# Performance work log

Measured on AMD Instinct MI355X. Metric: run time of the kernel, lower is better.

The kernel has to match this reference:

```python
import jax, jax.numpy as jnp
import numpy as np

N, E, H, ED, ND, OUT, L = 40000, 640000, 128, 128, 16, 3, 3


def setup_inputs() -> dict:
    key = jax.random.key(0)
    ks = jax.random.split(key, 16)
    s = 0.05  # weight init scale
    return {
        "x": jax.random.normal(ks[0], (N, ND), jnp.float32),
        "edge_index": jax.random.randint(ks[1], (2, E), 0, N, jnp.int32),
        "edge_attr": jax.random.normal(ks[2], (E, ED), jnp.float32),
        "e2n_W1": jax.random.normal(ks[3], (ED, H), jnp.float32) * s,
        "e2n_b1": jnp.zeros((H,), jnp.float32),
        "e2n_W2": jax.random.normal(ks[4], (H, H), jnp.float32) * s,
        "e2n_b2": jnp.zeros((H,), jnp.float32),
        "edge_W1": jax.random.normal(ks[5], (L, 2 * H + ED, H), jnp.float32) * s,
        "edge_b1": jnp.zeros((L, H), jnp.float32),
        "edge_W2": jax.random.normal(ks[6], (L, H, H), jnp.float32) * s,
        "edge_b2": jnp.zeros((L, H), jnp.float32),
        "node_W": jax.random.normal(ks[7], (L, H, H), jnp.float32) * s,
        "node_b": jnp.zeros((L, H), jnp.float32),
        "out_W1": jax.random.normal(ks[8], (H, H), jnp.float32) * s,
        "out_b1": jnp.zeros((H,), jnp.float32),
        "out_W2": jax.random.normal(ks[9], (H, OUT), jnp.float32) * s,
        "out_b2": jnp.zeros((OUT,), jnp.float32),
    }


def reference(x, edge_index, edge_attr, e2n_W1, e2n_b1, e2n_W2, e2n_b2,
              edge_W1, edge_b1, edge_W2, edge_b2, node_W, node_b,
              out_W1, out_b1, out_W2, out_b2):
    n = x.shape[0]
    src, dst = edge_index[0], edge_index[1]

    # edge_to_node_mlp then per-edge scatter-ADD into node features
    em = jax.nn.relu(edge_attr @ e2n_W1 + e2n_b1) @ e2n_W2 + e2n_b2  # [E,H]
    h = jax.ops.segment_sum(em, dst, num_segments=n)  # [N,H]

    # in-degree for mean aggregation (PyG aggr='mean'; empty nodes -> 0)
    cnt = jax.ops.segment_sum(jnp.ones((src.shape[0],), h.dtype), dst, num_segments=n)
    deg = jnp.maximum(cnt, 1.0)[:, None]  # [N,1]

    for l in range(edge_W1.shape[0]):
        feat = jnp.concatenate([h[dst], h[src], edge_attr], axis=-1)  # [E,2H+ED]
        m = jax.nn.relu(feat @ edge_W1[l] + edge_b1[l]) @ edge_W2[l] + edge_b2[l]
        agg = jax.ops.segment_sum(m, dst, num_segments=n) / deg  # scatter-mean
        h = jax.nn.relu(agg @ node_W[l] + node_b[l])

    return jax.nn.relu(h @ out_W1 + out_b1) @ out_W2 + out_b2  # [N,OUT]
```

## Files before the change

### kernel.cpp

```cpp
#include <hip/hip_runtime.h>
#include <hip/hip_bf16.h>

#define DEVINL __device__ __forceinline__

typedef float f32x4 __attribute__((ext_vector_type(4)));
typedef unsigned short u16x8 __attribute__((ext_vector_type(8)));
typedef __bf16 bf16x8 __attribute__((ext_vector_type(8)));

static constexpr int NN = 40000;
static constexpr int NE = 640000;
static constexpr int H  = 128;
static constexpr int NSCAN = 40;

static constexpr long O_HACC = 0;
static constexpr long O_H16  = 20480000;
static constexpr long O_DEG  = 30720000;
static constexpr long O_WP   = 30880000;
static constexpr long O_HDP  = 31600896;
static constexpr long O_HSP  = 41840896;
static constexpr long O_CNT  = 52080896;
static constexpr long O_LOC  = 52240896;
static constexpr long O_ROWP = 52400896;
static constexpr long O_CURS = 52560912;
static constexpr long O_BSUM = 52720912;
static constexpr long O_PERM = 52721168;
static constexpr long O_SRCS = 55281168;
static constexpr long O_DSTS = 57841168;
static constexpr long O_T16  = 60401168;
static constexpr long O_EA16 = 224241168;
static constexpr long NEED_T1 = O_EA16;
static constexpr long NEED_T2 = O_EA16 + (long)NE * H * 2;

__host__ __device__ inline const unsigned short* wpm(const unsigned short* wp, int m) {
  return wp + m * 16384;
}

DEVINL unsigned short f2bf(float f) {
  unsigned int u = __float_as_uint(f);
  u += 0x7fffu + ((u >> 16) & 1u);
  return (unsigned short)(u >> 16);
}
DEVINL float bf2f(unsigned short u) {
  return __uint_as_float(((unsigned int)u) << 16);
}

DEVINL f32x4 mfma16(u16x8 a, u16x8 b, f32x4 c) {
  return __builtin_amdgcn_mfma_f32_16x16x32_bf16(
      __builtin_bit_cast(bf16x8, a), __builtin_bit_cast(bf16x8, b), c, 0, 0, 0);
}

struct PrepPtrs { const float* p[18]; };

__global__ void prep_all(PrepPtrs pp, unsigned short* __restrict__ wp) {
  constexpr int MODE[18] = {0,1, 0,0,0, 0,0,0, 0,0,0, 1,1,1, 0,0,0, 0};
  int m = blockIdx.y;
  int idx = blockIdx.x * 256 + threadIdx.x;
  if (idx >= 16384) return;
  int j  = idx & 7, l = (idx >> 3) & 63, nb = (idx >> 9) & 7, ks = idx >> 12;
  int hi = l >> 4, lo = l & 15;
  int k = MODE[m] ? (4*ks + hi + 16*j) : (32*ks + 8*hi + j);
  int n = nb*16 + lo;
  wp[m * 16384 + idx] = f2bf(pp.p[m][k*128 + n]);
}

__global__ void hist_k(const int* __restrict__ dst, unsigned* __restrict__ cnt) {
  int e = blockIdx.x * 256 + threadIdx.x;
  atomicAdd(&cnt[dst[e]], 1u);
}

__global__ void scan1_k(const unsigned* __restrict__ cnt, unsigned* __restrict__ loc,
                        unsigned* __restrict__ bsum) {
  __shared__ unsigned sh[256];
  int t = threadIdx.x;
  int base = blockIdx.x * 1024 + t * 4;
  unsigned v[4]; unsigned s = 0;
  #pragma unroll
  for (int j = 0; j < 4; ++j) {
    v[j] = (base + j < NN) ? cnt[base + j] : 0u;
    s += v[j];
  }
  sh[t] = s; __syncthreads();
  #pragma unroll
  for (int off = 1; off < 256; off <<= 1) {
    unsigned y = (t >= off) ? sh[t - off] : 0u;
    __syncthreads();
    sh[t] += y;
    __syncthreads();
  }
  unsigned run = sh[t] - s;
  #pragma unroll
  for (int j = 0; j < 4; ++j) {
    if (base + j < NN) loc[base + j] = run;
    run += v[j];
  }
  if (t == 255) bsum[blockIdx.x] = sh[255];
}

__global__ void scan2_k(unsigned* __restrict__ bsum) {
  int t = threadIdx.x;
  unsigned orig = (t < NSCAN) ? bsum[t] : 0u;
  unsigned v = orig;
  #pragma unroll
  for (int off = 1; off < 64; off <<= 1) {
    unsigned y = __shfl_up(v, off);
    if (t >= off) v += y;
  }
  if (t < NSCAN) bsum[t] = v - orig;
}

__global__ void scan3_k(const unsigned* __restrict__ loc, const unsigned* __restrict__ bsum,
                        const unsigned* __restrict__ cnt, unsigned* __restrict__ rowPtr,
                        unsigned* __restrict__ cursor, float* __restrict__ deg_inv) {
  int i = blockIdx.x * 256 + threadIdx.x;
  if (i < NN) {
    unsigned r = loc[i] + bsum[i >> 10];
    rowPtr[i] = r;
    cursor[i] = r;
    deg_inv[i] = 1.0f / fmaxf((float)cnt[i], 1.0f);
  }
  if (i == NN) rowPtr[NN] = (unsigned)NE;
}

__global__ void scat_k(const int* __restrict__ src, const int* __restrict__ dst,
                       unsigned* __restrict__ cursor, unsigned* __restrict__ perm,
                       int* __restrict__ srcS, int* __restrict__ dstS) {
  int e = blockIdx.x * 256 + threadIdx.x;
  int d = dst[e];
  unsigned pos = atomicAdd(&cursor[d], 1u);
  perm[pos] = (unsigned)e;
  srcS[pos] = src[e];
  dstS[pos] = d;
}

__global__ void cvt_h0(const float* __restrict__ src, unsigned short* __restrict__ dst) {
  long i = ((long)blockIdx.x * 256 + threadIdx.x) * 8;
  f32x4 a = *(const f32x4*)(src + i);
  f32x4 b = *(const f32x4*)(src + i + 4);
  u16x8 t;
  #pragma unroll
  for (int j = 0; j < 4; ++j) { t[j] = f2bf(a[j]); t[4+j] = f2bf(b[j]); }
  *(u16x8*)(dst + i) = t;
}

__global__ __launch_bounds__(256) void node_xform(
    const unsigned short* __restrict__ h16,
    const unsigned short* __restrict__ wpa, const unsigned short* __restrict__ wpb,
    unsigned short* __restrict__ Hdp, unsigned short* __restrict__ Hsp) {
  const int tid = threadIdx.x;
  const int wave = tid >> 6, lane = tid & 63;
  const int hi = lane >> 4, lo = lane & 15;
  const int n0w = blockIdx.x * 256 + wave * 64;

  #pragma unroll
  for (int out = 0; out < 2; ++out) {
    const unsigned short* wp = out ? wpb : wpa;
    unsigned short* dp = out ? Hsp : Hdp;
    f32x4 acc[4][8];
    #pragma unroll
    for (int mf = 0; mf < 4; ++mf)
      #pragma unroll
      for (int nb = 0; nb < 8; ++nb) acc[mf][nb] = (f32x4)(0.0f);
    #pragma unroll
    for (int s = 0; s < 4; ++s) {
      u16x8 a[4];
      #pragma unroll
      for (int mf = 0; mf < 4; ++mf) {
        int n = n0w + 16 * mf + lo; if (n >= NN) n = NN - 1;
        a[mf] = *(const u16x8*)(h16 + (long)n * 128 + s * 32 + hi * 8);
      }
      #pragma unroll
      for (int nb = 0; nb < 8; ++nb) {
        u16x8 b = *(const u16x8*)(wp + ((s * 8 + nb) * 64 + lane) * 8);
        #pragma unroll
        for (int mf = 0; mf < 4; ++mf) acc[mf][nb] = mfma16(a[mf], b, acc[mf][nb]);
      }
    }
    #pragma unroll
    for (int mf = 0; mf < 4; ++mf)
      #pragma unroll
      for (int r = 0; r < 4; ++r) {
        int n = n0w + 16 * mf + 4 * hi + r;
        if (n < NN) {
          u16x8 pack;
          #pragma unroll
          for (int nb = 0; nb < 8; ++nb) pack[nb] = f2bf(acc[mf][nb][r]);
          *(u16x8*)(dp + (long)n * 128 + 8 * lo) = pack;
        }
      }
  }
}

template<int EAM, bool EAST, bool GATH>
__global__ __launch_bounds__(256, 2) void k12_pass(
    const float* __restrict__ ea32, unsigned short* __restrict__ ea16,
    const unsigned* __restrict__ perm,
    const unsigned short* __restrict__ w1p, const unsigned short* __restrict__ w2p,
    const float* __restrict__ b1, const float* __restrict__ b2,
    const unsigned short* __restrict__ Hdp, const unsigned short* __restrict__ Hsp,
    const int* __restrict__ srcS, const int* __restrict__ dstS,
    const float* __restrict__ deg_inv, float* __restrict__ hacc) {
  extern __shared__ char smem[];
  const int tid = threadIdx.x;
  const int wave = tid >> 6, lane = tid & 63;
  const int hi = lane >> 4, lo = lane & 15;

  const int nwg = gridDim.x;
  const int xcd = blockIdx.x & 7, bbase = blockIdx.x >> 3;
  const int qc = nwg >> 3, rc = nwg & 7;
  const int bid = (xcd < rc ? xcd * (qc + 1) : rc * (qc + 1) + (xcd - rc) * qc) + bbase;
  const long e0w = (long)bid * 256 + wave * 64;
  char* sstripe = smem + 65536 + wave * 4096;

  constexpr int LB = (EAM == 0 ? 8 : 4) + (GATH ? 8 : 0);

  unsigned pId[4];
  int dId[4], sId[4];
  float dsc[4];
  #pragma unroll
  for (int mf = 0; mf < 4; ++mf) {
    if (EAM == 0) pId[mf] = perm[e0w + 16 * mf + lo];
    dId[mf] = dstS[e0w + 16 * mf + lo];
    if (GATH) {
      sId[mf] = srcS[e0w + 16 * mf + lo];
      dsc[mf] = deg_inv[dId[mf]];
    }
  }

  float b1v[8], b2v[8];
  #pragma unroll
  for (int nb = 0; nb < 8; ++nb) { b1v[nb] = b1[nb * 16 + lo]; b2v[nb] = b2[nb * 16 + lo]; }

  u16x8 eaA[4], eaB[4], gdA[4], gsA[4], gdB[4], gsB[4];
  f32x4 efA[8], efB[8];

  auto issue = [&](int mf, u16x8 (&ea)[4], f32x4 (&ef)[8],
                   u16x8 (&gd)[4], u16x8 (&gs)[4]) {
    if (EAM == 1) {
      #pragma unroll
      for (int s = 0; s < 4; ++s) {
        const unsigned short* p = ea16 + (e0w + 16 * mf + lo) * 128 + s * 32 + hi * 8;
        asm volatile("global_load_dwordx4 %0, %1, off" : "=&v"(ea[s]) : "v"(p) : "memory");
      }
    } else {
      #pragma unroll
      for (int s = 0; s < 4; ++s) {
        const float* p = ea32 + (long)pId[mf] * 128 + s * 32 + hi * 8;
        asm volatile("global_load_dwordx4 %0, %1, off" : "=&v"(ef[2*s])   : "v"(p)     : "memory");
        asm volatile("global_load_dwordx4 %0, %1, off" : "=&v"(ef[2*s+1]) : "v"(p + 4) : "memory");
      }
    }
    if (GATH) {
      #pragma unroll
      for (int r = 0; r < 4; ++r) {
        int rd = __shfl(dId[mf], 4 * hi + r);
        int rs = __shfl(sId[mf], 4 * hi + r);
        const unsigned short* pd = Hdp + (long)rd * 128 + 8 * lo;
        const unsigned short* ps = Hsp + (long)rs * 128 + 8 * lo;
        asm volatile("global_load_dwordx4 %0, %1, off" : "=&v"(gd[r]) : "v"(pd) : "memory");
        asm volatile("global_load_dwordx4 %0, %1, off" : "=&v"(gs[r]) : "v"(ps) : "memory");
      }
    }
  };

  issue(0, eaA, efA, gdA, gsA);

  {
    const u16x8* g1 = (const u16x8*)w1p;
    u16x8* l1 = (u16x8*)smem;
    #pragma unroll
    for (int i = 0; i < 8; ++i) l1[i * 256 + tid] = g1[i * 256 + tid];
    const u16x8* g2 = (const u16x8*)w2p;
    u16x8* l2 = (u16x8*)(smem + 32768);
    #pragma unroll
    for (int i = 0; i < 8; ++i) l2[i * 256 + tid] = g2[i * 256 + tid];
  }
  __syncthreads();

  float runA = 0.0f, runB = 0.0f, scur = 1.0f;
  int dcur = -1;
  const int cA = 16 * ((2 * lane) & 7) + (lane >> 2);
  const int cB = 16 * ((2 * lane + 1) & 7) + (lane >> 2);

  #pragma unroll
  for (int mf = 0; mf < 4; ++mf) {
    u16x8 (&ea)[4] = (mf & 1) ? eaB : eaA;
    f32x4 (&ef)[8] = (mf & 1) ? efB : efA;
    u16x8 (&gd)[4] = (mf & 1) ? gdB : gdA;
    u16x8 (&gs)[4] = (mf & 1) ? gsB : gsA;
    if (mf < 3)
      issue(mf + 1, (mf & 1) ? eaA : eaB, (mf & 1) ? efA : efB,
            (mf & 1) ? gdA : gdB, (mf & 1) ? gsA : gsB);

    if (EAM == 1) {
      if (GATH) {
        asm volatile("s_waitcnt vmcnt(%12)"
          : "+v"(ea[0]), "+v"(ea[1]), "+v"(ea[2]), "+v"(ea[3]),
            "+v"(gd[0]), "+v"(gd[1]), "+v"(gd[2]), "+v"(gd[3]),
            "+v"(gs[0]), "+v"(gs[1]), "+v"(gs[2]), "+v"(gs[3])
          : "n"(mf < 3 ? LB : 0));
      } else {
        asm volatile("s_waitcnt vmcnt(%4)"
          : "+v"(ea[0]), "+v"(ea[1]), "+v"(ea[2]), "+v"(ea[3])
          : "n"(mf < 3 ? LB : 0));
      }
    } else if (GATH) {
      asm volatile("s_waitcnt vmcnt(%16)"
        : "+v"(ef[0]), "+v"(ef[1]), "+v"(ef[2]), "+v"(ef[3]),
          "+v"(ef[4]), "+v"(ef[5]), "+v"(ef[6]), "+v"(ef[7]),
          "+v"(gd[0]), "+v"(gd[1]), "+v"(gd[2]), "+v"(gd[3]),
          "+v"(gs[0]), "+v"(gs[1]), "+v"(gs[2]), "+v"(gs[3])
        : "n"(mf < 3 ? LB : 0));
    } else {
      asm volatile("s_waitcnt vmcnt(%8)"
        : "+v"(ef[0]), "+v"(ef[1]), "+v"(ef[2]), "+v"(ef[3]),
          "+v"(ef[4]), "+v"(ef[5]), "+v"(ef[6]), "+v"(ef[7])
        : "n"(mf < 3 ? LB : 0));
    }

    if (EAM == 0) {
      #pragma unroll
      for (int s = 0; s < 4; ++s) {
        u16x8 t;
        #pragma unroll
        for (int j = 0; j < 4; ++j) { t[j] = f2bf(ef[2*s][j]); t[4+j] = f2bf(ef[2*s+1][j]); }
        if (EAST)
          *(u16x8*)(ea16 + (e0w + 16 * mf + lo) * 128 + s * 32 + hi * 8) = t;
        ea[s] = t;
      }
    }

    f32x4 acc[8];
    #pragma unroll
    for (int nb = 0; nb < 8; ++nb) acc[nb] = (f32x4)(0.0f);
    #pragma unroll
    for (int s = 0; s < 4; ++s)
      #pragma unroll
      for (int nb = 0; nb < 8; ++nb) {
        u16x8 b = *(const u16x8*)(smem + ((s * 8 + nb) << 10) + (lane << 4));
        acc[nb] = mfma16(ea[s], b, acc[nb]);
      }
    if (GATH) {
      #pragma unroll
      for (int nb = 0; nb < 8; ++nb)
        #pragma unroll
        for (int r = 0; r < 4; ++r)
          acc[nb][r] += bf2f(gd[r][nb]) + bf2f(gs[r][nb]);
    }

    #pragma unroll
    for (int r = 0; r < 4; ++r) {
      int er = 4 * hi + r;
      u16x8 pack;
      #pragma unroll
      for (int nb = 0; nb < 8; ++nb)
        pack[nb] = f2bf(fmaxf(acc[nb][r] + b1v[nb], 0.0f));
      *(u16x8*)(sstripe + er * 256 + ((lo * 16) ^ ((er & 7) << 4))) = pack;
    }

    f32x4 acc2[8];
    #pragma unroll
    for (int nb = 0; nb < 8; ++nb) acc2[nb] = (f32x4)(0.0f);
    #pragma unroll
    for (int s2 = 0; s2 < 4; ++s2) {
      u16x8 a = *(const u16x8*)(sstripe + lo * 256 +
                                (((4 * s2 + hi) * 16) ^ ((lo & 7) << 4)));
      #pragma unroll
      for (int nb = 0; nb < 8; ++nb) {
        u16x8 b = *(const u16x8*)(smem + 32768 + ((s2 * 8 + nb) << 10) + (lane << 4));
        acc2[nb] = mfma16(a, b, acc2[nb]);
      }
    }

    #pragma unroll
    for (int r = 0; r < 4; ++r) {
      int er = 4 * hi + r;
      u16x8 pack;
      #pragma unroll
      for (int nb = 0; nb < 8; ++nb)
        pack[nb] = f2bf(acc2[nb][r] + b2v[nb]);
      *(u16x8*)(sstripe + er * 256 + ((lo * 16) ^ ((er & 7) << 4))) = pack;
    }

    #pragma unroll
    for (int er = 0; er < 16; ++er) {
      int d = __shfl(dId[mf], er);
      float s = GATH ? __shfl(dsc[mf], er) : 1.0f;
      if (d != dcur) {
        if (dcur >= 0) {
          unsafeAtomicAdd(&hacc[(long)dcur * 128 + cA], runA * scur);
          unsafeAtomicAdd(&hacc[(long)dcur * 128 + cB], runB * scur);
        }
        runA = 0.0f; runB = 0.0f; dcur = d; scur = s;
      }
      unsigned pr = *(const unsigned*)(sstripe + er * 256 +
                                       ((lane * 4) ^ ((er & 7) << 4)));
      runA += bf2f((unsigned short)(pr & 0xffffu));
      runB += bf2f((unsigned short)(pr >> 16));
    }
  }
  if (dcur >= 0) {
    unsafeAtomicAdd(&hacc[(long)dcur * 128 + cA], runA * scur);
    unsafeAtomicAdd(&hacc[(long)dcur * 128 + cB], runB * scur);
  }
}

__global__ __launch_bounds__(256) void node_pass(
    const float* __restrict__ agg, const unsigned short* __restrict__ wp,
    const float* __restrict__ bias, unsigned short* __restrict__ h16out) {
  __shared__ char smem[49152];
  const int tid = threadIdx.x;
  const int wave = tid >> 6, lane = tid & 63;
  const int hi = lane >> 4, lo = lane & 15;
  const int n0 = blockIdx.x * 64;
  const int r = tid >> 2, q = tid & 3;

  #pragma unroll
  for (int s = 0; s < 4; ++s) {
    f32x4 f0 = *(const f32x4*)(agg + (long)(n0 + r) * 128 + s * 32 + q * 8);
    f32x4 f1 = *(const f32x4*)(agg + (long)(n0 + r) * 128 + s * 32 + q * 8 + 4);
    u16x8 t;
    #pragma unroll
    for (int j = 0; j < 4; ++j) { t[j] = f2bf(f0[j]); t[4+j] = f2bf(f1[j]); }
    *(u16x8*)(smem + s * 4096 + (((r >> 4) * 64 + q * 16 + (r & 15)) << 4)) = t;
  }
  {
    const u16x8* g = (const u16x8*)wp;
    u16x8* l = (u16x8*)(smem + 16384);
    #pragma unroll
    for (int i = 0; i < 8; ++i) l[i * 256 + tid] = g[i * 256 + tid];
  }
  __syncthreads();

  f32x4 acc[8];
  #pragma unroll
  for (int nb = 0; nb < 8; ++nb) acc[nb] = (f32x4)(0.0f);
  #pragma unroll
  for (int s = 0; s < 4; ++s) {
    u16x8 a = *(const u16x8*)(smem + s * 4096 + wave * 1024 + (lane << 4));
    #pragma unroll
    for (int nb = 0; nb < 8; ++nb) {
      u16x8 b = *(const u16x8*)(smem + 16384 + ((s * 8 + nb) << 10) + (lane << 4));
      acc[nb] = mfma16(a, b, acc[nb]);
    }
  }
  float bv[8];
  #pragma unroll
  for (int nb = 0; nb < 8; ++nb) bv[nb] = bias[nb * 16 + lo];
  #pragma unroll
  for (int nb = 0; nb < 8; ++nb)
    #pragma unroll
    for (int rr = 0; rr < 4; ++rr) {
      int node = n0 + 16 * wave + 4 * hi + rr;
      float v = fmaxf(acc[nb][rr] + bv[nb], 0.0f);
      h16out[(long)node * 128 + nb * 16 + lo] = f2bf(v);
    }
}

__global__ __launch_bounds__(256) void out_pass(
    const unsigned short* __restrict__ h16, const unsigned short* __restrict__ wp,
    const float* __restrict__ ob1, const float* __restrict__ oW2,
    const float* __restrict__ ob2, float* __restrict__ out) {
  __shared__ char smem[49152];
  const int tid = threadIdx.x;
  const int wave = tid >> 6, lane = tid & 63;
  const int hi = lane >> 4, lo = lane & 15;
  const int n0 = blockIdx.x * 64;
  const int r = tid >> 2, q = tid & 3;

  #pragma unroll
  for (int s = 0; s < 4; ++s) {
    u16x8 t = *(const u16x8*)(h16 + (long)(n0 + r) * 128 + s * 32 + q * 8);
    *(u16x8*)(smem + s * 4096 + (((r >> 4) * 64 + q * 16 + (r & 15)) << 4)) = t;
  }
  {
    const u16x8* g = (const u16x8*)wp;
    u16x8* l = (u16x8*)(smem + 16384);
    #pragma unroll
    for (int i = 0; i < 8; ++i) l[i * 256 + tid] = g[i * 256 + tid];
  }
  __syncthreads();

  f32x4 acc[8];
  #pragma unroll
  for (int nb = 0; nb < 8; ++nb) acc[nb] = (f32x4)(0.0f);
  #pragma unroll
  for (int s = 0; s < 4; ++s) {
    u16x8 a = *(const u16x8*)(smem + s * 4096 + wave * 1024 + (lane << 4));
    #pragma unroll
    for (int nb = 0; nb < 8; ++nb) {
      u16x8 b = *(const u16x8*)(smem + 16384 + ((s * 8 + nb) << 10) + (lane << 4));
      acc[nb] = mfma16(a, b, acc[nb]);
    }
  }
  float b1v[8], w2v[8][3];
  #pragma unroll
  for (int nb = 0; nb < 8; ++nb) {
    b1v[nb] = ob1[nb * 16 + lo];
    #pragma unroll
    for (int o = 0; o < 3; ++o) w2v[nb][o] = oW2[(nb * 16 + lo) * 3 + o];
  }
  #pragma unroll
  for (int rr = 0; rr < 4; ++rr) {
    float p0 = 0.f, p1 = 0.f, p2 = 0.f;
    #pragma unroll
    for (int nb = 0; nb < 8; ++nb) {
      float t = fmaxf(acc[nb][rr] + b1v[nb], 0.0f);
      p0 += t * w2v[nb][0]; p1 += t * w2v[nb][1]; p2 += t * w2v[nb][2];
    }
    #pragma unroll
    for (int off = 1; off < 16; off <<= 1) {
      p0 += __shfl_xor(p0, off); p1 += __shfl_xor(p1, off); p2 += __shfl_xor(p2, off);
    }
    if (lo == 0) {
      int node = n0 + 16 * wave + 4 * hi + rr;
      out[(long)node * 3 + 0] = p0 + ob2[0];
      out[(long)node * 3 + 1] = p1 + ob2[1];
      out[(long)node * 3 + 2] = p2 + ob2[2];
    }
  }
}

extern "C" void kernel_launch(void* const* d_in, const int* in_sizes, int n_in,
                              void* d_out, int out_size, void* d_ws, size_t ws_size,
                              hipStream_t stream) {
  const int*   ei     = (const int*)d_in[1];
  const int*   srcIds = ei;
  const int*   dstIds = ei + NE;
  const float* ea     = (const float*)d_in[2];
  const float* e2nb1  = (const float*)d_in[4];
  const float* e2nb2  = (const float*)d_in[6];
  const float* eW1    = (const float*)d_in[7];
  const float* eb1    = (const float*)d_in[8];
  const float* eW2    = (const float*)d_in[9];
  const float* eb2    = (const float*)d_in[10];
  const float* nW     = (const float*)d_in[11];
  const float* nb_    = (const float*)d_in[12];
  const float* ob1    = (const float*)d_in[14];
  const float* oW2    = (const float*)d_in[15];
  const float* ob2    = (const float*)d_in[16];
  float* out = (float*)d_out;

  char* ws = (char*)d_ws;
  float* hacc = (float*)(ws + O_HACC);
  unsigned short* h16 = (unsigned short*)(ws + O_H16);
  float* deg_inv = (float*)(ws + O_DEG);
  unsigned short* wp = (unsigned short*)(ws + O_WP);
  unsigned short* Hdp = (unsigned short*)(ws + O_HDP);
  unsigned short* Hsp = (unsigned short*)(ws + O_HSP);
  unsigned* cnt    = (unsigned*)(ws + O_CNT);
  unsigned* loc    = (unsigned*)(ws + O_LOC);
  unsigned* rowPtr = (unsigned*)(ws + O_ROWP);
  unsigned* cursor = (unsigned*)(ws + O_CURS);
  unsigned* bsum   = (unsigned*)(ws + O_BSUM);
  unsigned* perm   = (unsigned*)(ws + O_PERM);
  int* srcS        = (int*)(ws + O_SRCS);
  int* dstS        = (int*)(ws + O_DSTS);
  unsigned short* ea16 = (unsigned short*)(ws + O_EA16);
  const bool tier2 = ws_size >= (size_t)NEED_T2;

  PrepPtrs pp;
  pp.p[0] = (const float*)d_in[3];
  pp.p[1] = (const float*)d_in[5];
  for (int l = 0; l < 3; ++l) {
    pp.p[2 + 3*l] = eW1 + l * 49152;
    pp.p[3 + 3*l] = eW1 + l * 49152 + 16384;
    pp.p[4 + 3*l] = eW1 + l * 49152 + 32768;
    pp.p[11 + l]  = eW2 + l * 16384;
    pp.p[14 + l]  = nW  + l * 16384;
  }
  pp.p[17] = (const float*)d_in[13];

  prep_all<<<dim3(64, 18), 256, 0, stream>>>(pp, wp);

  hipMemsetAsync(cnt, 0, (size_t)NN * 4, stream);
  hist_k<<<NE / 256, 256, 0, stream>>>(dstIds, cnt);
  scan1_k<<<NSCAN, 256, 0, stream>>>(cnt, loc, bsum);
  scan2_k<<<1, 64, 0, stream>>>(bsum);
  scan3_k<<<(NN + 256) / 256, 256, 0, stream>>>(loc, bsum, cnt, rowPtr, cursor, deg_inv);
  scat_k<<<NE / 256, 256, 0, stream>>>(srcIds, dstIds, cursor, perm, srcS, dstS);

  hipMemsetAsync(hacc, 0, (size_t)NN * H * 4, stream);
  if (tier2)
    k12_pass<0, true, false><<<NE / 256, 256, 81920, stream>>>(
        ea, ea16, perm, wpm(wp, 0), wpm(wp, 1), e2nb1, e2nb2,
        nullptr, nullptr, srcS, dstS, deg_inv, hacc);
  else
    k12_pass<0, false, false><<<NE / 256, 256, 81920, stream>>>(
        ea, nullptr, perm, wpm(wp, 0), wpm(wp, 1), e2nb1, e2nb2,
        nullptr, nullptr, srcS, dstS, deg_inv, hacc);
  cvt_h0<<<NN * H / (256 * 8), 256, 0, stream>>>(hacc, h16);

  for (int l = 0; l < 3; ++l) {
    node_xform<<<(NN + 255) / 256, 256, 0, stream>>>(
        h16, wpm(wp, 2 + 3*l), wpm(wp, 3 + 3*l), Hdp, Hsp);
    hipMemsetAsync(hacc, 0, (size_t)NN * H * 4, stream);
    if (tier2)
      k12_pass<1, false, true><<<NE / 256, 256, 81920, stream>>>(
          ea, ea16, perm, wpm(wp, 4 + 3*l), wpm(wp, 11 + l),
          eb1 + l * 128, eb2 + l * 128, Hdp, Hsp, srcS, dstS, deg_inv, hacc);
    else
      k12_pass<0, false, true><<<NE / 256, 256, 81920, stream>>>(
          ea, nullptr, perm, wpm(wp, 4 + 3*l), wpm(wp, 11 + l),
          eb1 + l * 128, eb2 + l * 128, Hdp, Hsp, srcS, dstS, deg_inv, hacc);
    node_pass<<<NN / 64, 256, 0, stream>>>(hacc, wpm(wp, 14 + l),
                                           nb_ + l * 128, h16);
  }

  out_pass<<<NN / 64, 256, 0, stream>>>(h16, wpm(wp, 17), ob1, oW2, ob2, out);
}
```

Before: 633.3 us.

## Fuse node update with next-layer node transform and fold h0 conversion

```diff
diff --git a/kernel.cpp b/kernel.cpp
--- a/kernel.cpp
+++ b/kernel.cpp
@@ -26,9 +26,7 @@
 static constexpr long O_PERM = 52721168;
 static constexpr long O_SRCS = 55281168;
 static constexpr long O_DSTS = 57841168;
-static constexpr long O_T16  = 60401168;
 static constexpr long O_EA16 = 224241168;
-static constexpr long NEED_T1 = O_EA16;
 static constexpr long NEED_T2 = O_EA16 + (long)NE * H * 2;
 
 __host__ __device__ inline const unsigned short* wpm(const unsigned short* wp, int m) {
@@ -49,10 +47,10 @@
       __builtin_bit_cast(bf16x8, a), __builtin_bit_cast(bf16x8, b), c, 0, 0, 0);
 }
 
-struct PrepPtrs { const float* p[18]; };
+struct PrepPtrs { const float* p[22]; };
 
 __global__ void prep_all(PrepPtrs pp, unsigned short* __restrict__ wp) {
-  constexpr int MODE[18] = {0,1, 0,0,0, 0,0,0, 0,0,0, 1,1,1, 0,0,0, 0};
+  constexpr int MODE[22] = {0,1, 0,0,0, 0,0,0, 0,0,0, 1,1,1, 0,0,0, 0, 1,1,1,1};
   int m = blockIdx.y;
   int idx = blockIdx.x * 256 + threadIdx.x;
   if (idx >= 16384) return;
@@ -132,18 +130,8 @@
   dstS[pos] = d;
 }
 
-__global__ void cvt_h0(const float* __restrict__ src, unsigned short* __restrict__ dst) {
-  long i = ((long)blockIdx.x * 256 + threadIdx.x) * 8;
-  f32x4 a = *(const f32x4*)(src + i);
-  f32x4 b = *(const f32x4*)(src + i + 4);
-  u16x8 t;
-  #pragma unroll
-  for (int j = 0; j < 4; ++j) { t[j] = f2bf(a[j]); t[4+j] = f2bf(b[j]); }
-  *(u16x8*)(dst + i) = t;
-}
-
 __global__ __launch_bounds__(256) void node_xform(
-    const unsigned short* __restrict__ h16,
+    const float* __restrict__ hsrc,
     const unsigned short* __restrict__ wpa, const unsigned short* __restrict__ wpb,
     unsigned short* __restrict__ Hdp, unsigned short* __restrict__ Hsp) {
   const int tid = threadIdx.x;
@@ -151,6 +139,20 @@
   const int hi = lane >> 4, lo = lane & 15;
   const int n0w = blockIdx.x * 256 + wave * 64;
 
+  u16x8 a[4][4];
+  #pragma unroll
+  for (int s = 0; s < 4; ++s)
+    #pragma unroll
+    for (int mf = 0; mf < 4; ++mf) {
+      int n = n0w + 16 * mf + lo; if (n >= NN) n = NN - 1;
+      f32x4 f0 = *(const f32x4*)(hsrc + (long)n * 128 + s * 32 + hi * 8);
+      f32x4 f1 = *(const f32x4*)(hsrc + (long)n * 128 + s * 32 + hi * 8 + 4);
+      u16x8 t;
+      #pragma unroll
+      for (int j = 0; j < 4; ++j) { t[j] = f2bf(f0[j]); t[4+j] = f2bf(f1[j]); }
+      a[s][mf] = t;
+    }
+
   #pragma unroll
   for (int out = 0; out < 2; ++out) {
     const unsigned short* wp = out ? wpb : wpa;
@@ -161,20 +163,13 @@
       #pragma unroll
       for (int nb = 0; nb < 8; ++nb) acc[mf][nb] = (f32x4)(0.0f);
     #pragma unroll
-    for (int s = 0; s < 4; ++s) {
-      u16x8 a[4];
-      #pragma unroll
-      for (int mf = 0; mf < 4; ++mf) {
-        int n = n0w + 16 * mf + lo; if (n >= NN) n = NN - 1;
-        a[mf] = *(const u16x8*)(h16 + (long)n * 128 + s * 32 + hi * 8);
-      }
+    for (int s = 0; s < 4; ++s)
       #pragma unroll
       for (int nb = 0; nb < 8; ++nb) {
         u16x8 b = *(const u16x8*)(wp + ((s * 8 + nb) * 64 + lane) * 8);
         #pragma unroll
-        for (int mf = 0; mf < 4; ++mf) acc[mf][nb] = mfma16(a[mf], b, acc[mf][nb]);
-      }
-    }
+        for (int mf = 0; mf < 4; ++mf) acc[mf][nb] = mfma16(a[s][mf], b, acc[mf][nb]);
+      }
     #pragma unroll
     for (int mf = 0; mf < 4; ++mf)
       #pragma unroll
@@ -187,6 +182,106 @@
           *(u16x8*)(dp + (long)n * 128 + 8 * lo) = pack;
         }
       }
+  }
+}
+
+template<bool XF>
+__global__ __launch_bounds__(256) void node_fused(
+    const float* __restrict__ agg, const unsigned short* __restrict__ wn,
+    const float* __restrict__ bias,
+    const unsigned short* __restrict__ w1aK, const unsigned short* __restrict__ w1bK,
+    unsigned short* __restrict__ h16out,
+    unsigned short* __restrict__ Hdp, unsigned short* __restrict__ Hsp) {
+  __shared__ char smem[16384];
+  const int tid = threadIdx.x;
+  const int wave = tid >> 6, lane = tid & 63;
+  const int hi = lane >> 4, lo = lane & 15;
+  const int n0w = blockIdx.x * 256 + wave * 64;
+  char* sstripe = smem + wave * 4096;
+
+  float bv[8];
+  #pragma unroll
+  for (int nb = 0; nb < 8; ++nb) bv[nb] = bias[nb * 16 + lo];
+
+  f32x4 acc[4][8];
+  #pragma unroll
+  for (int mf = 0; mf < 4; ++mf)
+    #pragma unroll
+    for (int nb = 0; nb < 8; ++nb) acc[mf][nb] = (f32x4)(0.0f);
+
+  #pragma unroll
+  for (int s = 0; s < 4; ++s) {
+    u16x8 a[4];
+    #pragma unroll
+    for (int mf = 0; mf < 4; ++mf) {
+      int n = n0w + 16 * mf + lo; if (n >= NN) n = NN - 1;
+      f32x4 f0 = *(const f32x4*)(agg + (long)n * 128 + s * 32 + hi * 8);
+      f32x4 f1 = *(const f32x4*)(agg + (long)n * 128 + s * 32 + hi * 8 + 4);
+      u16x8 t;
+      #pragma unroll
+      for (int j = 0; j < 4; ++j) { t[j] = f2bf(f0[j]); t[4+j] = f2bf(f1[j]); }
+      a[mf] = t;
+    }
+    #pragma unroll
+    for (int nb = 0; nb < 8; ++nb) {
+      u16x8 b = *(const u16x8*)(wn + ((s * 8 + nb) * 64 + lane) * 8);
+      #pragma unroll
+      for (int mf = 0; mf < 4; ++mf) acc[mf][nb] = mfma16(a[mf], b, acc[mf][nb]);
+    }
+  }
+
+  #pragma unroll
+  for (int mf = 0; mf < 4; ++mf) {
+    u16x8 hp[4];
+    #pragma unroll
+    for (int r = 0; r < 4; ++r)
+      #pragma unroll
+      for (int nb = 0; nb < 8; ++nb)
+        hp[r][nb] = f2bf(fmaxf(acc[mf][nb][r] + bv[nb], 0.0f));
+
+    #pragma unroll
+    for (int nb = 0; nb < 8; ++nb)
+      #pragma unroll
+      for (int r = 0; r < 4; ++r) {
+        int n = n0w + 16 * mf + 4 * hi + r;
+        if (n < NN) h16out[(long)n * 128 + nb * 16 + lo] = hp[r][nb];
+      }
+
+    if (XF) {
+      #pragma unroll
+      for (int r = 0; r < 4; ++r) {
+        int er = 4 * hi + r;
+        *(u16x8*)(sstripe + er * 256 + ((lo * 16) ^ ((er & 7) << 4))) = hp[r];
+      }
+      #pragma unroll
+      for (int out = 0; out < 2; ++out) {
+        const unsigned short* wb = out ? w1bK : w1aK;
+        unsigned short* dp = out ? Hsp : Hdp;
+        f32x4 a2[8];
+        #pragma unroll
+        for (int nb = 0; nb < 8; ++nb) a2[nb] = (f32x4)(0.0f);
+        #pragma unroll
+        for (int s2 = 0; s2 < 4; ++s2) {
+          u16x8 a = *(const u16x8*)(sstripe + lo * 256 +
+                                    (((4 * s2 + hi) * 16) ^ ((lo & 7) << 4)));
+          #pragma unroll
+          for (int nb = 0; nb < 8; ++nb) {
+            u16x8 b = *(const u16x8*)(wb + ((s2 * 8 + nb) * 64 + lane) * 8);
+            a2[nb] = mfma16(a, b, a2[nb]);
+          }
+        }
+        #pragma unroll
+        for (int r = 0; r < 4; ++r) {
+          int n = n0w + 16 * mf + 4 * hi + r;
+          if (n < NN) {
+            u16x8 pack;
+            #pragma unroll
+            for (int nb = 0; nb < 8; ++nb) pack[nb] = f2bf(a2[nb][r]);
+            *(u16x8*)(dp + (long)n * 128 + 8 * lo) = pack;
+          }
+        }
+      }
+    }
   }
 }
 
@@ -212,6 +307,7 @@
   char* sstripe = smem + 65536 + wave * 4096;
 
   constexpr int LB = (EAM == 0 ? 8 : 4) + (GATH ? 8 : 0);
+  constexpr int SB = (EAM == 0 && EAST) ? 4 : 0;
 
   unsigned pId[4];
   int dId[4], sId[4];
@@ -232,6 +328,7 @@
 
   u16x8 eaA[4], eaB[4], gdA[4], gsA[4], gdB[4], gsB[4];
   f32x4 efA[8], efB[8];
+  u16x8 mp0[4], mp1[4], mp2[4], mp3[4];
 
   auto issue = [&](int mf, u16x8 (&ea)[4], f32x4 (&ef)[8],
                    u16x8 (&gd)[4], u16x8 (&gs)[4]) {
@@ -275,11 +372,6 @@
     for (int i = 0; i < 8; ++i) l2[i * 256 + tid] = g2[i * 256 + tid];
   }
   __syncthreads();
-
-  float runA = 0.0f, runB = 0.0f, scur = 1.0f;
-  int dcur = -1;
-  const int cA = 16 * ((2 * lane) & 7) + (lane >> 2);
-  const int cB = 16 * ((2 * lane + 1) & 7) + (lane >> 2);
 
   #pragma unroll
   for (int mf = 0; mf < 4; ++mf) {
@@ -297,11 +389,11 @@
           : "+v"(ea[0]), "+v"(ea[1]), "+v"(ea[2]), "+v"(ea[3]),
             "+v"(gd[0]), "+v"(gd[1]), "+v"(gd[2]), "+v"(gd[3]),
             "+v"(gs[0]), "+v"(gs[1]), "+v"(gs[2]), "+v"(gs[3])
-          : "n"(mf < 3 ? LB : 0));
+          : "n"((mf < 3 ? LB : 0) + (mf > 0 ? SB : 0)));
       } else {
         asm volatile("s_waitcnt vmcnt(%4)"
           : "+v"(ea[0]), "+v"(ea[1]), "+v"(ea[2]), "+v"(ea[3])
-          : "n"(mf < 3 ? LB : 0));
+          : "n"((mf < 3 ? LB : 0) + (mf > 0 ? SB : 0)));
       }
     } else if (GATH) {
       asm volatile("s_waitcnt vmcnt(%16)"
@@ -309,12 +401,12 @@
           "+v"(ef[4]), "+v"(ef[5]), "+v"(ef[6]), "+v"(ef[7]),
           "+v"(gd[0]), "+v"(gd[1]), "+v"(gd[2]), "+v"(gd[3]),
           "+v"(gs[0]), "+v"(gs[1]), "+v"(gs[2]), "+v"(gs[3])
-        : "n"(mf < 3 ? LB : 0));
+        : "n"((mf < 3 ? LB : 0) + (mf > 0 ? SB : 0)));
     } else {
       asm volatile("s_waitcnt vmcnt(%8)"
         : "+v"(ef[0]), "+v"(ef[1]), "+v"(ef[2]), "+v"(ef[3]),
           "+v"(ef[4]), "+v"(ef[5]), "+v"(ef[6]), "+v"(ef[7])
-        : "n"(mf < 3 ? LB : 0));
+        : "n"((mf < 3 ? LB : 0) + (mf > 0 ? SB : 0)));
     }
 
     if (EAM == 0) {
@@ -357,9 +449,8 @@
       *(u16x8*)(sstripe + er * 256 + ((lo * 16) ^ ((er & 7) << 4))) = pack;
     }
 
-    f32x4 acc2[8];
-    #pragma unroll
-    for (int nb = 0; nb < 8; ++nb) acc2[nb] = (f32x4)(0.0f);
+    #pragma unroll
+    for (int nb = 0; nb < 8; ++nb) acc[nb] = (f32x4)(0.0f);
     #pragma unroll
     for (int s2 = 0; s2 < 4; ++s2) {
       u16x8 a = *(const u16x8*)(sstripe + lo * 256 +
@@ -367,20 +458,31 @@
       #pragma unroll
       for (int nb = 0; nb < 8; ++nb) {
         u16x8 b = *(const u16x8*)(smem + 32768 + ((s2 * 8 + nb) << 10) + (lane << 4));
-        acc2[nb] = mfma16(a, b, acc2[nb]);
-      }
-    }
-
+        acc[nb] = mfma16(a, b, acc[nb]);
+      }
+    }
+
+    u16x8 (&mp)[4] = (mf == 0) ? mp0 : (mf == 1) ? mp1 : (mf == 2) ? mp2 : mp3;
+    #pragma unroll
+    for (int r = 0; r < 4; ++r)
+      #pragma unroll
+      for (int nb = 0; nb < 8; ++nb)
+        mp[r][nb] = f2bf(acc[nb][r] + b2v[nb]);
+  }
+
+  float runA = 0.0f, runB = 0.0f, scur = 1.0f;
+  int dcur = -1;
+  const int cA = 16 * ((2 * lane) & 7) + (lane >> 2);
+  const int cB = 16 * ((2 * lane + 1) & 7) + (lane >> 2);
+
+  #pragma unroll
+  for (int mf = 0; mf < 4; ++mf) {
+    u16x8 (&mp)[4] = (mf == 0) ? mp0 : (mf == 1) ? mp1 : (mf == 2) ? mp2 : mp3;
     #pragma unroll
     for (int r = 0; r < 4; ++r) {
       int er = 4 * hi + r;
-      u16x8 pack;
-      #pragma unroll
-      for (int nb = 0; nb < 8; ++nb)
-        pack[nb] = f2bf(acc2[nb][r] + b2v[nb]);
-      *(u16x8*)(sstripe + er * 256 + ((lo * 16) ^ ((er & 7) << 4))) = pack;
-    }
-
+      *(u16x8*)(sstripe + er * 256 + ((lo * 16) ^ ((er & 7) << 4))) = mp[r];
+    }
     #pragma unroll
     for (int er = 0; er < 16; ++er) {
       int d = __shfl(dId[mf], er);
@@ -402,58 +504,6 @@
     unsafeAtomicAdd(&hacc[(long)dcur * 128 + cA], runA * scur);
     unsafeAtomicAdd(&hacc[(long)dcur * 128 + cB], runB * scur);
   }
-}
-
-__global__ __launch_bounds__(256) void node_pass(
-    const float* __restrict__ agg, const unsigned short* __restrict__ wp,
-    const float* __restrict__ bias, unsigned short* __restrict__ h16out) {
-  __shared__ char smem[49152];
-  const int tid = threadIdx.x;
-  const int wave = tid >> 6, lane = tid & 63;
-  const int hi = lane >> 4, lo = lane & 15;
-  const int n0 = blockIdx.x * 64;
-  const int r = tid >> 2, q = tid & 3;
-
-  #pragma unroll
-  for (int s = 0; s < 4; ++s) {
-    f32x4 f0 = *(const f32x4*)(agg + (long)(n0 + r) * 128 + s * 32 + q * 8);
-    f32x4 f1 = *(const f32x4*)(agg + (long)(n0 + r) * 128 + s * 32 + q * 8 + 4);
-    u16x8 t;
-    #pragma unroll
-    for (int j = 0; j < 4; ++j) { t[j] = f2bf(f0[j]); t[4+j] = f2bf(f1[j]); }
-    *(u16x8*)(smem + s * 4096 + (((r >> 4) * 64 + q * 16 + (r & 15)) << 4)) = t;
-  }
-  {
-    const u16x8* g = (const u16x8*)wp;
-    u16x8* l = (u16x8*)(smem + 16384);
-    #pragma unroll
-    for (int i = 0; i < 8; ++i) l[i * 256 + tid] = g[i * 256 + tid];
-  }
-  __syncthreads();
-
-  f32x4 acc[8];
-  #pragma unroll
-  for (int nb = 0; nb < 8; ++nb) acc[nb] = (f32x4)(0.0f);
-  #pragma unroll
-  for (int s = 0; s < 4; ++s) {
-    u16x8 a = *(const u16x8*)(smem + s * 4096 + wave * 1024 + (lane << 4));
-    #pragma unroll
-    for (int nb = 0; nb < 8; ++nb) {
-      u16x8 b = *(const u16x8*)(smem + 16384 + ((s * 8 + nb) << 10) + (lane << 4));
-      acc[nb] = mfma16(a, b, acc[nb]);
-    }
-  }
-  float bv[8];
-  #pragma unroll
-  for (int nb = 0; nb < 8; ++nb) bv[nb] = bias[nb * 16 + lo];
-  #pragma unroll
-  for (int nb = 0; nb < 8; ++nb)
-    #pragma unroll
-    for (int rr = 0; rr < 4; ++rr) {
-      int node = n0 + 16 * wave + 4 * hi + rr;
-      float v = fmaxf(acc[nb][rr] + bv[nb], 0.0f);
-      h16out[(long)node * 128 + nb * 16 + lo] = f2bf(v);
-    }
 }
 
 __global__ __launch_bounds__(256) void out_pass(
@@ -569,8 +619,12 @@
     pp.p[14 + l]  = nW  + l * 16384;
   }
   pp.p[17] = (const float*)d_in[13];
-
-  prep_all<<<dim3(64, 18), 256, 0, stream>>>(pp, wp);
+  pp.p[18] = eW1 + 1 * 49152;
+  pp.p[19] = eW1 + 1 * 49152 + 16384;
+  pp.p[20] = eW1 + 2 * 49152;
+  pp.p[21] = eW1 + 2 * 49152 + 16384;
+
+  prep_all<<<dim3(64, 22), 256, 0, stream>>>(pp, wp);
 
   hipMemsetAsync(cnt, 0, (size_t)NN * 4, stream);
   hist_k<<<NE / 256, 256, 0, stream>>>(dstIds, cnt);
@@ -588,11 +642,11 @@
     k12_pass<0, false, false><<<NE / 256, 256, 81920, stream>>>(
         ea, nullptr, perm, wpm(wp, 0), wpm(wp, 1), e2nb1, e2nb2,
         nullptr, nullptr, srcS, dstS, deg_inv, hacc);
-  cvt_h0<<<NN * H / (256 * 8), 256, 0, stream>>>(hacc, h16);
+
+  node_xform<<<(NN + 255) / 256, 256, 0, stream>>>(
+      hacc, wpm(wp, 2), wpm(wp, 3), Hdp, Hsp);
 
   for (int l = 0; l < 3; ++l) {
-    node_xform<<<(NN + 255) / 256, 256, 0, stream>>>(
-        h16, wpm(wp, 2 + 3*l), wpm(wp, 3 + 3*l), Hdp, Hsp);
     hipMemsetAsync(hacc, 0, (size_t)NN * H * 4, stream);
     if (tier2)
       k12_pass<1, false, true><<<NE / 256, 256, 81920, stream>>>(
@@ -602,8 +656,14 @@
       k12_pass<0, false, true><<<NE / 256, 256, 81920, stream>>>(
           ea, nullptr, perm, wpm(wp, 4 + 3*l), wpm(wp, 11 + l),
           eb1 + l * 128, eb2 + l * 128, Hdp, Hsp, srcS, dstS, deg_inv, hacc);
-    node_pass<<<NN / 64, 256, 0, stream>>>(hacc, wpm(wp, 14 + l),
-                                           nb_ + l * 128, h16);
+    if (l < 2)
+      node_fused<true><<<(NN + 255) / 256, 256, 0, stream>>>(
+          hacc, wpm(wp, 14 + l), nb_ + l * 128,
+          wpm(wp, 18 + 2*l), wpm(wp, 19 + 2*l), h16, Hdp, Hsp);
+    else
+      node_fused<false><<<(NN + 255) / 256, 256, 0, stream>>>(
+          hacc, wpm(wp, 14 + l), nb_ + l * 128,
+          nullptr, nullptr, h16, nullptr, nullptr);
   }
 
   out_pass<<<NN / 64, 256, 0, stream>>>(h16, wpm(wp, 17), ob1, oW2, ob2, out);
```

Result: slower. 702.4 us (+10.9%).
